# Performance work log

Measured on AMD Instinct MI355X. Metric: run time of the kernel, lower is better.

Reference implementation:

```python
import jax, jax.numpy as jnp
import numpy as np

# Mamba hyperparams (mamba_ssm defaults for d_model=128)
D_MODEL = 128
DEPTH = 8
D_INNER = 256   # expand=2
D_STATE = 16
D_CONV = 4
DT_RANK = 8     # ceil(D_MODEL/16)
EPS = 1e-5


def setup_inputs() -> dict:
    key = jax.random.key(0)
    ks = jax.random.split(key, 8)
    B, H, W = 1, 48, 48
    s = lambda k, shape, sc=0.02: jax.random.normal(k, shape, jnp.float32) * sc
    return {
        "x": jax.random.normal(ks[0], (B, D_MODEL, H, W), jnp.float32),
        "W_in": s(ks[1], (DEPTH, D_MODEL, 2 * D_INNER)),
        "conv_w": s(ks[2], (DEPTH, D_INNER, D_CONV), 0.2),
        "conv_b": jnp.zeros((DEPTH, D_INNER), jnp.float32),
        "W_xproj": s(ks[3], (DEPTH, D_INNER, DT_RANK + 2 * D_STATE)),
        "W_dt": s(ks[4], (DEPTH, DT_RANK, D_INNER), 0.1),
        "b_dt": jnp.full((DEPTH, D_INNER), -4.6, jnp.float32),  # softplus ~= 0.01
        "A_log": jnp.broadcast_to(
            jnp.log(jnp.arange(1, D_STATE + 1, dtype=jnp.float32)),
            (DEPTH, D_INNER, D_STATE)).copy(),
        "D_skip": jnp.ones((DEPTH, D_INNER), jnp.float32),
        "W_out": s(ks[5], (DEPTH, D_INNER, D_MODEL)),
        "rms_w": jnp.ones((DEPTH, D_MODEL), jnp.float32),
    }


def _rmsnorm(x, w):
    return x * jax.lax.rsqrt(jnp.mean(x * x, axis=-1, keepdims=True) + EPS) * w


def _mamba_layer(x, Wi, cw, cb, Wx, Wdt, bdt, Alog, Dp, Wo):
    # x: [B, L, D_MODEL]
    B, L, _ = x.shape
    xz = x @ Wi                                   # [B, L, 2*d_inner]
    xi, z = jnp.split(xz, 2, axis=-1)
    # causal depthwise conv1d, kernel D_CONV
    xp = jnp.pad(xi, ((0, 0), (D_CONV - 1, 0), (0, 0)))
    xc = sum(xp[:, k:k + L, :] * cw[:, k] for k in range(D_CONV)) + cb
    xc = jax.nn.silu(xc)                          # [B, L, d_inner]
    dbl = xc @ Wx                                 # [B, L, dt_rank + 2*d_state]
    dt_r = dbl[..., :DT_RANK]
    Bs = dbl[..., DT_RANK:DT_RANK + D_STATE]      # [B, L, d_state]
    Cs = dbl[..., DT_RANK + D_STATE:]
    dt = jax.nn.softplus(dt_r @ Wdt + bdt)        # [B, L, d_inner]
    A = -jnp.exp(Alog)                            # [d_inner, d_state]
    dA = jnp.exp(dt[..., None] * A)               # [B, L, d_inner, d_state]
    dBx = (dt * xc)[..., None] * Bs[:, :, None, :]
    # linear recurrence h_t = dA_t * h_{t-1} + dBx_t via parallel scan
    def comb(l, r):
        al, bl = l
        ar, br = r
        return ar * al, ar * bl + br
    _, h = jax.lax.associative_scan(comb, (dA, dBx), axis=1)
    y = jnp.einsum('blds,bls->bld', h, Cs) + Dp * xc
    y = y * jax.nn.silu(z)
    return y @ Wo                                 # [B, L, D_MODEL]


def reference(x, W_in, conv_w, conv_b, W_xproj, W_dt, b_dt, A_log, D_skip, W_out, rms_w):
    B, C, H, W = x.shape
    seq = x.reshape(B, C, H * W).transpose(0, 2, 1)  # [B, L, C]
    for l in range(DEPTH):
        seq = _mamba_layer(seq, W_in[l], conv_w[l], conv_b[l], W_xproj[l],
                           W_dt[l], b_dt[l], A_log[l], D_skip[l], W_out[l])
        seq = _rmsnorm(seq, rms_w[l])
    return seq.reshape(B, H, W, C).transpose(0, 3, 1, 2)
```

## Files before the change

### kernel.cpp

```cpp
#include <hip/hip_runtime.h>
#include <math.h>

#define LSEQ 2304
#define DM 128
#define DI 256
#define DS 16
#define RK 8
#define NCH 576
#define CLEN 4
#define NG 24
#define GS 24
#define NSI (DI*DS)
#define EPSF 1e-5f

__device__ __forceinline__ float silu_f(float s) { return s / (1.f + __expf(-s)); }
__device__ __forceinline__ float softplus_f(float x) { return (x > 20.f) ? x : log1pf(__expf(x)); }

template<bool FIRST>
__global__ __launch_bounds__(256, 4)
void k_in(const float* __restrict__ seq, const float* __restrict__ x0,
          const float* __restrict__ Wi,
          const float* __restrict__ cw, const float* __restrict__ cbias,
          float* __restrict__ xc_g, float* __restrict__ sz_g) {
    __shared__ float As[19 * 128];
    const int l0 = blockIdx.x * 16;
    const int half = blockIdx.y & 1;
    const bool isZ = blockIdx.y >= 2;
    const int tid = threadIdx.x;

    if (FIRST) {
        const int rlo = isZ ? 3 : 0;
        for (int idx = tid + rlo * 128; idx < 19 * 128; idx += 256) {
            const int r = idx >> 7, cc = idx & 127;
            const int l = l0 - 3 + r;
            As[idx] = (l >= 0) ? x0[cc * LSEQ + l] : 0.f;
        }
    } else if (!isZ) {
        for (int idx = tid; idx < 19 * 32; idx += 256) {
            const int r = idx >> 5, cq = (idx & 31) * 4;
            const int l = l0 - 3 + r;
            const float4 v = (l >= 0) ? *(const float4*)&seq[l * DM + cq]
                                      : make_float4(0.f, 0.f, 0.f, 0.f);
            *(float4*)&As[r * 128 + cq] = v;
        }
    } else {
        for (int idx = tid; idx < 16 * 32; idx += 256) {
            const int r = 3 + (idx >> 5), cq = (idx & 31) * 4;
            *(float4*)&As[r * 128 + cq] =
                *(const float4*)&seq[(l0 - 3 + r) * DM + cq];
        }
    }
    __syncthreads();

    const int c = tid & 127;
    const int rg = tid >> 7;
    const int d = half * 128 + c;

    if (!isZ) {
        float ax[11];
#pragma unroll
        for (int r = 0; r < 11; ++r) ax[r] = 0.f;
        for (int k4 = 0; k4 < 32; ++k4) {
            float bv[4];
#pragma unroll
            for (int u = 0; u < 4; ++u) bv[u] = Wi[(k4 * 4 + u) * 512 + d];
#pragma unroll
            for (int r = 0; r < 11; ++r) {
                const float4 a4 = *(const float4*)&As[(rg * 8 + r) * 128 + k4 * 4];
                ax[r] += a4.x * bv[0] + a4.y * bv[1] + a4.z * bv[2] + a4.w * bv[3];
            }
        }
        const float w0 = cw[d * 4 + 0], w1 = cw[d * 4 + 1];
        const float w2 = cw[d * 4 + 2], w3 = cw[d * 4 + 3];
        const float cbv = cbias[d];
#pragma unroll
        for (int rr = 0; rr < 8; ++rr) {
            const float v = silu_f(cbv + w0 * ax[rr] + w1 * ax[rr + 1] +
                                   w2 * ax[rr + 2] + w3 * ax[rr + 3]);
            xc_g[(l0 + rg * 8 + rr) * DI + d] = v;
        }
    } else {
        float az[8];
#pragma unroll
        for (int r = 0; r < 8; ++r) az[r] = 0.f;
        for (int k4 = 0; k4 < 32; ++k4) {
            float bv[4];
#pragma unroll
            for (int u = 0; u < 4; ++u) bv[u] = Wi[(k4 * 4 + u) * 512 + 256 + d];
#pragma unroll
            for (int r = 0; r < 8; ++r) {
                const float4 a4 = *(const float4*)&As[(rg * 8 + r + 3) * 128 + k4 * 4];
                az[r] += a4.x * bv[0] + a4.y * bv[1] + a4.z * bv[2] + a4.w * bv[3];
            }
        }
#pragma unroll
        for (int rr = 0; rr < 8; ++rr)
            sz_g[(l0 + rg * 8 + rr) * DI + d] = silu_f(az[rr]);
    }
}

__global__ __launch_bounds__(256, 4)
void k_mid2(const float* __restrict__ xc_g,
            const float* __restrict__ Wx,
            const float* __restrict__ Wdt, const float* __restrict__ bdt,
            const float* __restrict__ Alog,
            float* __restrict__ dbl_g, float* __restrict__ dts_g,
            float* __restrict__ S) {
    __shared__ float xcs[CLEN * 256];
    __shared__ float part[4 * 160];
    __shared__ float dtrs[CLEN * 8];
    __shared__ float dbls[CLEN * 32];
    const int c = blockIdx.x;
    const int l0 = c * CLEN;
    const int tid = threadIdx.x;
    const int d = tid;

    ((float4*)xcs)[tid] = ((const float4*)&xc_g[l0 * DI])[tid];
    __syncthreads();

    for (int task = tid; task < 640; task += 256) {
        const int kc = task / 160;
        const int o = task - kc * 160;
        const int r = o / 40, j = o - r * 40;
        const float* xr = &xcs[r * 256 + kc * 64];
        const float* wp = &Wx[(kc * 64) * 40 + j];
        float acc = 0.f;
#pragma unroll 8
        for (int k = 0; k < 64; ++k) acc += xr[k] * wp[k * 40];
        part[kc * 160 + o] = acc;
    }
    __syncthreads();
    if (tid < 160) {
        const float acc = part[tid] + part[160 + tid] + part[320 + tid] + part[480 + tid];
        const int r = tid / 40, j = tid - r * 40;
        dbl_g[(l0 + r) * 40 + j] = acc;
        if (j < RK) dtrs[r * 8 + j] = acc;
        else dbls[r * 32 + (j - 8)] = acc;
    }
    __syncthreads();

    float dtv[CLEN], xcv[CLEN];
    {
        float wdt[8];
#pragma unroll
        for (int q = 0; q < 8; ++q) wdt[q] = Wdt[q * DI + d];
        const float bdv = bdt[d];
#pragma unroll
        for (int r = 0; r < CLEN; ++r) {
            float acc = bdv;
#pragma unroll
            for (int q = 0; q < 8; ++q) acc += dtrs[r * 8 + q] * wdt[q];
            dtv[r] = softplus_f(acc);
            xcv[r] = xcs[r * 256 + d];
        }
    }
    dts_g[c * DI + d] = dtv[0] + dtv[1] + dtv[2] + dtv[3];

    float A[16], hs[16];
#pragma unroll
    for (int v = 0; v < 4; ++v) {
        const float4 a4 = *(const float4*)&Alog[d * DS + v * 4];
        A[v * 4 + 0] = -__expf(a4.x);
        A[v * 4 + 1] = -__expf(a4.y);
        A[v * 4 + 2] = -__expf(a4.z);
        A[v * 4 + 3] = -__expf(a4.w);
    }
#pragma unroll
    for (int s = 0; s < 16; ++s) hs[s] = 0.f;
#pragma unroll
    for (int t = 0; t < CLEN; ++t) {
        const float dtt = dtv[t];
        const float uv = dtt * xcv[t];
        const float* Brow = &dbls[t * 32];
#pragma unroll
        for (int s = 0; s < 16; ++s) {
            const float e = __expf(dtt * A[s]);
            hs[s] = e * hs[s] + uv * Brow[s];
        }
    }
    const int base = c * NSI + d * DS;
#pragma unroll
    for (int v = 0; v < 4; ++v) {
        *(float4*)&S[base + v * 4] =
            make_float4(hs[v * 4], hs[v * 4 + 1], hs[v * 4 + 2], hs[v * 4 + 3]);
    }
}

__global__ __launch_bounds__(256, 4)
void k_carry1(float* __restrict__ S, const float* __restrict__ dts,
              const float* __restrict__ Alog,
              float* __restrict__ dtspre,
              float* __restrict__ Pg, float* __restrict__ Sg) {
    const int g = blockIdx.x;
    const int i = blockIdx.y * 256 + threadIdx.x;
    const int d = i >> 4;
    const float Av = -__expf(Alog[i]);
    float G = 0.f, cd = 0.f;
    const int base = g * GS * NSI + i;
    const int c0 = g * GS;
#pragma unroll 8
    for (int k = 0; k < GS; ++k) {
        const int idx = base + k * NSI;
        const float dtsv = dts[(c0 + k) * DI + d];
        if ((i & 15) == 0) dtspre[(c0 + k) * DI + d] = cd;
        const float p = __expf(Av * dtsv);
        const float s = S[idx];
        S[idx] = G;
        G = p * G + s;
        cd += dtsv;
    }
    Pg[g * NSI + i] = __expf(Av * cd);
    Sg[g * NSI + i] = G;
}

__global__ __launch_bounds__(256, 4)
void k_carry2(const float* __restrict__ Pg, float* __restrict__ Sg) {
    const int i = blockIdx.x * 256 + threadIdx.x;
    float G = 0.f;
#pragma unroll 8
    for (int g = 0; g < NG; ++g) {
        const int idx = g * NSI + i;
        const float p = Pg[idx];
        const float s = Sg[idx];
        Sg[idx] = G;
        G = p * G + s;
    }
}

template<bool LAST>
__global__ __launch_bounds__(256, 3)
void k_tail(const float* __restrict__ xc_g, const float* __restrict__ dbl_g,
            const float* __restrict__ Alog, const float* __restrict__ Sloc,
            const float* __restrict__ dtspre, const float* __restrict__ Gc,
            const float* __restrict__ Dp, const float* __restrict__ sz_g,
            const float* __restrict__ Wdt, const float* __restrict__ bdt,
            const float* __restrict__ Wo, const float* __restrict__ rmsw,
            float* __restrict__ seq, float* __restrict__ out) {
    __shared__ float dbls[CLEN * 40];
    __shared__ float Ys[CLEN * 256];
    __shared__ float partO[4 * CLEN * 128];
    __shared__ float Os[CLEN * 129];
    __shared__ float red[CLEN * 32];
    __shared__ float scaleS[CLEN];
    const int c = blockIdx.x;
    const int g = c / GS;
    const int l0 = c * CLEN;
    const int tid = threadIdx.x;
    const int d = tid;

    if (tid < CLEN * 40) dbls[tid] = dbl_g[l0 * 40 + tid];

    float A[16], h[16];
    const float cdts = dtspre[c * DI + d];
#pragma unroll
    for (int v = 0; v < 4; ++v) {
        const float4 a4 = *(const float4*)&Alog[d * DS + v * 4];
        A[v * 4 + 0] = -__expf(a4.x);
        A[v * 4 + 1] = -__expf(a4.y);
        A[v * 4 + 2] = -__expf(a4.z);
        A[v * 4 + 3] = -__expf(a4.w);
        const float4 s4 = *(const float4*)&Sloc[c * NSI + d * DS + v * 4];
        const float4 g4 = *(const float4*)&Gc[g * NSI + d * DS + v * 4];
        h[v * 4 + 0] = s4.x + __expf(A[v * 4 + 0] * cdts) * g4.x;
        h[v * 4 + 1] = s4.y + __expf(A[v * 4 + 1] * cdts) * g4.y;
        h[v * 4 + 2] = s4.z + __expf(A[v * 4 + 2] * cdts) * g4.z;
        h[v * 4 + 3] = s4.w + __expf(A[v * 4 + 3] * cdts) * g4.w;
    }
    float xcv[CLEN], szv[CLEN];
#pragma unroll
    for (int r = 0; r < CLEN; ++r) {
        xcv[r] = xc_g[(l0 + r) * DI + d];
        szv[r] = sz_g[(l0 + r) * DI + d];
    }
    const float dskip = Dp[d];
    __syncthreads();

    float dtv[CLEN];
    {
        float wdt[8];
#pragma unroll
        for (int q = 0; q < 8; ++q) wdt[q] = Wdt[q * DI + d];
        const float bdv = bdt[d];
#pragma unroll
        for (int r = 0; r < CLEN; ++r) {
            float acc = bdv;
#pragma unroll
            for (int q = 0; q < 8; ++q) acc += dbls[r * 40 + q] * wdt[q];
            dtv[r] = softplus_f(acc);
        }
    }
#pragma unroll
    for (int t = 0; t < CLEN; ++t) {
        const float dtt = dtv[t];
        const float uv = dtt * xcv[t];
        const float* Brow = &dbls[t * 40 + 8];
        const float* Crow = &dbls[t * 40 + 24];
        float sum = 0.f;
#pragma unroll
        for (int s = 0; s < 16; ++s) {
            const float e = __expf(dtt * A[s]);
            h[s] = e * h[s] + uv * Brow[s];
            sum += h[s] * Crow[s];
        }
        Ys[t * 256 + d] = (sum + dskip * xcv[t]) * szv[t];
    }
    __syncthreads();

    {
        const int ccp = tid & 63;
        const int kg = tid >> 6;
        float acc[CLEN][2];
#pragma unroll
        for (int r = 0; r < CLEN; ++r) { acc[r][0] = 0.f; acc[r][1] = 0.f; }
        const float* wp = &Wo[(kg * 64) * DM + ccp * 2];
        const float* yp = &Ys[kg * 64];
#pragma unroll 8
        for (int k = 0; k < 64; ++k) {
            const float2 w2 = *(const float2*)(wp + k * DM);
#pragma unroll
            for (int r = 0; r < CLEN; ++r) {
                const float yv = yp[r * 256 + k];
                acc[r][0] += yv * w2.x;
                acc[r][1] += yv * w2.y;
            }
        }
#pragma unroll
        for (int r = 0; r < CLEN; ++r) {
            partO[(kg * CLEN + r) * 128 + ccp * 2 + 0] = acc[r][0];
            partO[(kg * CLEN + r) * 128 + ccp * 2 + 1] = acc[r][1];
        }
        __syncthreads();
        for (int idx = tid; idx < CLEN * 128; idx += 256) {
            const int r = idx >> 7, cc = idx & 127;
            Os[r * 129 + cc] = partO[(0 * CLEN + r) * 128 + cc] +
                               partO[(1 * CLEN + r) * 128 + cc] +
                               partO[(2 * CLEN + r) * 128 + cc] +
                               partO[(3 * CLEN + r) * 128 + cc];
        }
        __syncthreads();
    }

    if (tid < CLEN * 32) {
        const int r = tid >> 5, part = tid & 31;
        float ss = 0.f;
#pragma unroll
        for (int i = 0; i < 4; ++i) {
            const float v = Os[r * 129 + part * 4 + i];
            ss += v * v;
        }
        red[tid] = ss;
    }
    __syncthreads();
    if (tid < CLEN) {
        float ss = 0.f;
#pragma unroll
        for (int p = 0; p < 32; ++p) ss += red[tid * 32 + p];
        scaleS[tid] = rsqrtf(ss * (1.f / DM) + EPSF);
    }
    __syncthreads();
    if (LAST) {
        for (int idx = tid; idx < CLEN * DM; idx += 256) {
            const int r = idx >> 7, cc = idx & 127;
            out[cc * LSEQ + (l0 + r)] = Os[r * 129 + cc] * scaleS[r] * rmsw[cc];
        }
    } else {
        for (int idx = tid; idx < CLEN * DM; idx += 256) {
            const int r = idx >> 7, cc = idx & 127;
            seq[(l0 + r) * DM + cc] = Os[r * 129 + cc] * scaleS[r] * rmsw[cc];
        }
    }
}

extern "C" void kernel_launch(void* const* d_in, const int* in_sizes, int n_in,
                              void* d_out, int out_size, void* d_ws, size_t ws_size,
                              hipStream_t stream) {
    const float* x    = (const float*)d_in[0];
    const float* W_in = (const float*)d_in[1];
    const float* cw   = (const float*)d_in[2];
    const float* cb   = (const float*)d_in[3];
    const float* Wx   = (const float*)d_in[4];
    const float* Wdt  = (const float*)d_in[5];
    const float* bdt  = (const float*)d_in[6];
    const float* Alog = (const float*)d_in[7];
    const float* Dp   = (const float*)d_in[8];
    const float* Wo   = (const float*)d_in[9];
    const float* rmsw = (const float*)d_in[10];
    float* out = (float*)d_out;

    float* ws      = (float*)d_ws;
    float* seq     = ws; ws += LSEQ * DM;
    float* szb     = ws; ws += LSEQ * DI;
    float* xcb     = ws; ws += LSEQ * DI;
    float* dblb    = ws; ws += LSEQ * 40;
    float* dtsb    = ws; ws += NCH * DI;
    float* dtspreb = ws; ws += NCH * DI;
    float* Sb      = ws; ws += NCH * NSI;
    float* Pgb     = ws; ws += NG * NSI;
    float* Sgb     = ws; ws += NG * NSI;

    for (int layer = 0; layer < 8; ++layer) {
        const float* Wi_l   = W_in + (size_t)layer * DM * 512;
        const float* cw_l   = cw   + (size_t)layer * DI * 4;
        const float* cb_l   = cb   + (size_t)layer * DI;
        const float* Wx_l   = Wx   + (size_t)layer * DI * 40;
        const float* Wdt_l  = Wdt  + (size_t)layer * RK * DI;
        const float* bdt_l  = bdt  + (size_t)layer * DI;
        const float* Alog_l = Alog + (size_t)layer * DI * DS;
        const float* Dp_l   = Dp   + (size_t)layer * DI;
        const float* Wo_l   = Wo   + (size_t)layer * DI * DM;
        const float* rmsw_l = rmsw + (size_t)layer * DM;

        if (layer == 0)
            k_in<true><<<dim3(144, 4), 256, 0, stream>>>(seq, x, Wi_l, cw_l, cb_l,
                                                         xcb, szb);
        else
            k_in<false><<<dim3(144, 4), 256, 0, stream>>>(seq, x, Wi_l, cw_l, cb_l,
                                                          xcb, szb);

        k_mid2<<<NCH, 256, 0, stream>>>(xcb, Wx_l, Wdt_l, bdt_l, Alog_l,
                                        dblb, dtsb, Sb);

        k_carry1<<<dim3(NG, 16), 256, 0, stream>>>(Sb, dtsb, Alog_l,
                                                   dtspreb, Pgb, Sgb);
        k_carry2<<<16, 256, 0, stream>>>(Pgb, Sgb);

        if (layer == 7)
            k_tail<true><<<NCH, 256, 0, stream>>>(xcb, dblb, Alog_l, Sb, dtspreb,
                                                  Sgb, Dp_l, szb, Wdt_l, bdt_l,
                                                  Wo_l, rmsw_l, seq, out);
        else
            k_tail<false><<<NCH, 256, 0, stream>>>(xcb, dblb, Alog_l, Sb, dtspreb,
                                                   Sgb, Dp_l, szb, Wdt_l, bdt_l,
                                                   Wo_l, rmsw_l, seq, out);
    }
}
```

Before: 574.8 us.

## Fuse input projection with chunk-scan front, drop carry2 by folding group prefix into tail

```diff
diff --git a/kernel.cpp b/kernel.cpp
--- a/kernel.cpp
+++ b/kernel.cpp
@@ -8,9 +8,11 @@
 #define RK 8
 #define NCH 576
 #define CLEN 4
-#define NG 24
-#define GS 24
+#define NG 8
+#define GS 72
 #define NSI (DI*DS)
+#define TROWS 8
+#define NT (LSEQ/TROWS)
 #define EPSF 1e-5f
 
 __device__ __forceinline__ float silu_f(float s) { return s / (1.f + __expf(-s)); }
@@ -18,25 +20,36 @@
 
 template<bool FIRST>
 __global__ __launch_bounds__(256, 4)
-void k_in(const float* __restrict__ seq, const float* __restrict__ x0,
-          const float* __restrict__ Wi,
-          const float* __restrict__ cw, const float* __restrict__ cbias,
-          float* __restrict__ xc_g, float* __restrict__ sz_g) {
-    __shared__ float As[19 * 128];
-    const int l0 = blockIdx.x * 16;
-    const int half = blockIdx.y & 1;
-    const bool isZ = blockIdx.y >= 2;
+void k_front(const float* __restrict__ seq, const float* __restrict__ x0,
+             const float* __restrict__ Wi,
+             const float* __restrict__ cw, const float* __restrict__ cbias,
+             const float* __restrict__ Wx,
+             const float* __restrict__ Wdt, const float* __restrict__ bdt,
+             const float* __restrict__ Alog,
+             float* __restrict__ xc_g, float* __restrict__ sz_g,
+             float* __restrict__ dbl_g, float* __restrict__ dts_g,
+             float* __restrict__ S) {
+    __shared__ float As[11 * 128];
+    __shared__ float xcs[TROWS * 256];
+    __shared__ float part[2 * 4 * 160];
+    __shared__ float dtrs[TROWS * 8];
+    __shared__ float dbls[TROWS * 32];
+
+    const int tile = blockIdx.x;
+    const int l0 = tile * TROWS;
+    const bool isZ = blockIdx.y == 1;
     const int tid = threadIdx.x;
+    const int d = tid;
 
     if (FIRST) {
         const int rlo = isZ ? 3 : 0;
-        for (int idx = tid + rlo * 128; idx < 19 * 128; idx += 256) {
+        for (int idx = tid + rlo * 128; idx < 11 * 128; idx += 256) {
             const int r = idx >> 7, cc = idx & 127;
             const int l = l0 - 3 + r;
             As[idx] = (l >= 0) ? x0[cc * LSEQ + l] : 0.f;
         }
     } else if (!isZ) {
-        for (int idx = tid; idx < 19 * 32; idx += 256) {
+        for (int idx = tid; idx < 11 * 32; idx += 256) {
             const int r = idx >> 5, cq = (idx & 31) * 4;
             const int l = l0 - 3 + r;
             const float4 v = (l >= 0) ? *(const float4*)&seq[l * DM + cq]
@@ -44,7 +57,7 @@
             *(float4*)&As[r * 128 + cq] = v;
         }
     } else {
-        for (int idx = tid; idx < 16 * 32; idx += 256) {
+        for (int idx = tid; idx < 8 * 32; idx += 256) {
             const int r = 3 + (idx >> 5), cq = (idx & 31) * 4;
             *(float4*)&As[r * 128 + cq] =
                 *(const float4*)&seq[(l0 - 3 + r) * DM + cq];
@@ -52,24 +65,40 @@
     }
     __syncthreads();
 
-    const int c = tid & 127;
-    const int rg = tid >> 7;
-    const int d = half * 128 + c;
-
-    if (!isZ) {
-        float ax[11];
-#pragma unroll
-        for (int r = 0; r < 11; ++r) ax[r] = 0.f;
+    if (isZ) {
+        float az[8];
+#pragma unroll
+        for (int r = 0; r < 8; ++r) az[r] = 0.f;
         for (int k4 = 0; k4 < 32; ++k4) {
             float bv[4];
 #pragma unroll
-            for (int u = 0; u < 4; ++u) bv[u] = Wi[(k4 * 4 + u) * 512 + d];
-#pragma unroll
-            for (int r = 0; r < 11; ++r) {
-                const float4 a4 = *(const float4*)&As[(rg * 8 + r) * 128 + k4 * 4];
-                ax[r] += a4.x * bv[0] + a4.y * bv[1] + a4.z * bv[2] + a4.w * bv[3];
+            for (int u = 0; u < 4; ++u) bv[u] = Wi[(k4 * 4 + u) * 512 + 256 + d];
+#pragma unroll
+            for (int r = 0; r < 8; ++r) {
+                const float4 a4 = *(const float4*)&As[(r + 3) * 128 + k4 * 4];
+                az[r] += a4.x * bv[0] + a4.y * bv[1] + a4.z * bv[2] + a4.w * bv[3];
             }
         }
+#pragma unroll
+        for (int rr = 0; rr < 8; ++rr)
+            sz_g[(l0 + rr) * DI + d] = silu_f(az[rr]);
+        return;
+    }
+
+    float ax[11];
+#pragma unroll
+    for (int r = 0; r < 11; ++r) ax[r] = 0.f;
+    for (int k4 = 0; k4 < 32; ++k4) {
+        float bv[4];
+#pragma unroll
+        for (int u = 0; u < 4; ++u) bv[u] = Wi[(k4 * 4 + u) * 512 + d];
+#pragma unroll
+        for (int r = 0; r < 11; ++r) {
+            const float4 a4 = *(const float4*)&As[r * 128 + k4 * 4];
+            ax[r] += a4.x * bv[0] + a4.y * bv[1] + a4.z * bv[2] + a4.w * bv[3];
+        }
+    }
+    {
         const float w0 = cw[d * 4 + 0], w1 = cw[d * 4 + 1];
         const float w2 = cw[d * 4 + 2], w3 = cw[d * 4 + 3];
         const float cbv = cbias[d];
@@ -77,86 +106,42 @@
         for (int rr = 0; rr < 8; ++rr) {
             const float v = silu_f(cbv + w0 * ax[rr] + w1 * ax[rr + 1] +
                                    w2 * ax[rr + 2] + w3 * ax[rr + 3]);
-            xc_g[(l0 + rg * 8 + rr) * DI + d] = v;
-        }
-    } else {
-        float az[8];
-#pragma unroll
-        for (int r = 0; r < 8; ++r) az[r] = 0.f;
-        for (int k4 = 0; k4 < 32; ++k4) {
-            float bv[4];
-#pragma unroll
-            for (int u = 0; u < 4; ++u) bv[u] = Wi[(k4 * 4 + u) * 512 + 256 + d];
-#pragma unroll
-            for (int r = 0; r < 8; ++r) {
-                const float4 a4 = *(const float4*)&As[(rg * 8 + r + 3) * 128 + k4 * 4];
-                az[r] += a4.x * bv[0] + a4.y * bv[1] + a4.z * bv[2] + a4.w * bv[3];
-            }
-        }
-#pragma unroll
-        for (int rr = 0; rr < 8; ++rr)
-            sz_g[(l0 + rg * 8 + rr) * DI + d] = silu_f(az[rr]);
-    }
-}
-
-__global__ __launch_bounds__(256, 4)
-void k_mid2(const float* __restrict__ xc_g,
-            const float* __restrict__ Wx,
-            const float* __restrict__ Wdt, const float* __restrict__ bdt,
-            const float* __restrict__ Alog,
-            float* __restrict__ dbl_g, float* __restrict__ dts_g,
-            float* __restrict__ S) {
-    __shared__ float xcs[CLEN * 256];
-    __shared__ float part[4 * 160];
-    __shared__ float dtrs[CLEN * 8];
-    __shared__ float dbls[CLEN * 32];
-    const int c = blockIdx.x;
-    const int l0 = c * CLEN;
-    const int tid = threadIdx.x;
-    const int d = tid;
-
-    ((float4*)xcs)[tid] = ((const float4*)&xc_g[l0 * DI])[tid];
-    __syncthreads();
-
-    for (int task = tid; task < 640; task += 256) {
-        const int kc = task / 160;
-        const int o = task - kc * 160;
+            xcs[rr * 256 + d] = v;
+            xc_g[(l0 + rr) * DI + d] = v;
+        }
+    }
+    __syncthreads();
+
+    for (int task = tid; task < 1280; task += 256) {
+        const int q = task / 640;
+        const int rem = task - q * 640;
+        const int kc = rem / 160;
+        const int o = rem - kc * 160;
         const int r = o / 40, j = o - r * 40;
-        const float* xr = &xcs[r * 256 + kc * 64];
+        const float* xr = &xcs[(q * 4 + r) * 256 + kc * 64];
         const float* wp = &Wx[(kc * 64) * 40 + j];
         float acc = 0.f;
 #pragma unroll 8
         for (int k = 0; k < 64; ++k) acc += xr[k] * wp[k * 40];
-        part[kc * 160 + o] = acc;
-    }
-    __syncthreads();
-    if (tid < 160) {
-        const float acc = part[tid] + part[160 + tid] + part[320 + tid] + part[480 + tid];
-        const int r = tid / 40, j = tid - r * 40;
-        dbl_g[(l0 + r) * 40 + j] = acc;
-        if (j < RK) dtrs[r * 8 + j] = acc;
-        else dbls[r * 32 + (j - 8)] = acc;
-    }
-    __syncthreads();
-
-    float dtv[CLEN], xcv[CLEN];
-    {
-        float wdt[8];
-#pragma unroll
-        for (int q = 0; q < 8; ++q) wdt[q] = Wdt[q * DI + d];
-        const float bdv = bdt[d];
-#pragma unroll
-        for (int r = 0; r < CLEN; ++r) {
-            float acc = bdv;
-#pragma unroll
-            for (int q = 0; q < 8; ++q) acc += dtrs[r * 8 + q] * wdt[q];
-            dtv[r] = softplus_f(acc);
-            xcv[r] = xcs[r * 256 + d];
-        }
-    }
-    dts_g[c * DI + d] = dtv[0] + dtv[1] + dtv[2] + dtv[3];
-
-    float A[16], hs[16];
+        part[(q * 4 + kc) * 160 + o] = acc;
+    }
+    __syncthreads();
+    for (int idx = tid; idx < 320; idx += 256) {
+        const int q = idx / 160, o = idx - q * 160;
+        const float acc = part[(q * 4 + 0) * 160 + o] + part[(q * 4 + 1) * 160 + o] +
+                          part[(q * 4 + 2) * 160 + o] + part[(q * 4 + 3) * 160 + o];
+        const int r = o / 40, j = o - r * 40;
+        dbl_g[(l0 + q * 4 + r) * 40 + j] = acc;
+        if (j < RK) dtrs[(q * 4 + r) * 8 + j] = acc;
+        else        dbls[(q * 4 + r) * 32 + (j - 8)] = acc;
+    }
+    __syncthreads();
+
+    float wdt[8];
+#pragma unroll
+    for (int q8 = 0; q8 < 8; ++q8) wdt[q8] = Wdt[q8 * DI + d];
+    const float bdv = bdt[d];
+    float A[16];
 #pragma unroll
     for (int v = 0; v < 4; ++v) {
         const float4 a4 = *(const float4*)&Alog[d * DS + v * 4];
@@ -166,38 +151,54 @@
         A[v * 4 + 3] = -__expf(a4.w);
     }
 #pragma unroll
-    for (int s = 0; s < 16; ++s) hs[s] = 0.f;
-#pragma unroll
-    for (int t = 0; t < CLEN; ++t) {
-        const float dtt = dtv[t];
-        const float uv = dtt * xcv[t];
-        const float* Brow = &dbls[t * 32];
-#pragma unroll
-        for (int s = 0; s < 16; ++s) {
-            const float e = __expf(dtt * A[s]);
-            hs[s] = e * hs[s] + uv * Brow[s];
-        }
-    }
-    const int base = c * NSI + d * DS;
-#pragma unroll
-    for (int v = 0; v < 4; ++v) {
-        *(float4*)&S[base + v * 4] =
-            make_float4(hs[v * 4], hs[v * 4 + 1], hs[v * 4 + 2], hs[v * 4 + 3]);
+    for (int q = 0; q < 2; ++q) {
+        const int c = tile * 2 + q;
+        float dtv[CLEN], xcv[CLEN];
+#pragma unroll
+        for (int r = 0; r < CLEN; ++r) {
+            float acc = bdv;
+#pragma unroll
+            for (int k = 0; k < 8; ++k) acc += dtrs[(q * 4 + r) * 8 + k] * wdt[k];
+            dtv[r] = softplus_f(acc);
+            xcv[r] = xcs[(q * 4 + r) * 256 + d];
+        }
+        dts_g[c * DI + d] = dtv[0] + dtv[1] + dtv[2] + dtv[3];
+
+        float hs[16];
+#pragma unroll
+        for (int s = 0; s < 16; ++s) hs[s] = 0.f;
+#pragma unroll
+        for (int t = 0; t < CLEN; ++t) {
+            const float dtt = dtv[t];
+            const float uv = dtt * xcv[t];
+            const float* Brow = &dbls[(q * 4 + t) * 32];
+#pragma unroll
+            for (int s = 0; s < 16; ++s) {
+                const float e = __expf(dtt * A[s]);
+                hs[s] = e * hs[s] + uv * Brow[s];
+            }
+        }
+        const int base = c * NSI + d * DS;
+#pragma unroll
+        for (int v = 0; v < 4; ++v) {
+            *(float4*)&S[base + v * 4] =
+                make_float4(hs[v * 4], hs[v * 4 + 1], hs[v * 4 + 2], hs[v * 4 + 3]);
+        }
     }
 }
 
 __global__ __launch_bounds__(256, 4)
-void k_carry1(float* __restrict__ S, const float* __restrict__ dts,
-              const float* __restrict__ Alog,
-              float* __restrict__ dtspre,
-              float* __restrict__ Pg, float* __restrict__ Sg) {
+void k_carry(float* __restrict__ S, const float* __restrict__ dts,
+             const float* __restrict__ Alog,
+             float* __restrict__ dtspre,
+             float* __restrict__ Pg, float* __restrict__ Sg) {
     const int g = blockIdx.x;
     const int i = blockIdx.y * 256 + threadIdx.x;
     const int d = i >> 4;
     const float Av = -__expf(Alog[i]);
     float G = 0.f, cd = 0.f;
-    const int base = g * GS * NSI + i;
     const int c0 = g * GS;
+    const int base = c0 * NSI + i;
 #pragma unroll 8
     for (int k = 0; k < GS; ++k) {
         const int idx = base + k * NSI;
@@ -213,25 +214,12 @@
     Sg[g * NSI + i] = G;
 }
 
-__global__ __launch_bounds__(256, 4)
-void k_carry2(const float* __restrict__ Pg, float* __restrict__ Sg) {
-    const int i = blockIdx.x * 256 + threadIdx.x;
-    float G = 0.f;
-#pragma unroll 8
-    for (int g = 0; g < NG; ++g) {
-        const int idx = g * NSI + i;
-        const float p = Pg[idx];
-        const float s = Sg[idx];
-        Sg[idx] = G;
-        G = p * G + s;
-    }
-}
-
 template<bool LAST>
 __global__ __launch_bounds__(256, 3)
 void k_tail(const float* __restrict__ xc_g, const float* __restrict__ dbl_g,
             const float* __restrict__ Alog, const float* __restrict__ Sloc,
-            const float* __restrict__ dtspre, const float* __restrict__ Gc,
+            const float* __restrict__ dtspre,
+            const float* __restrict__ Pg, const float* __restrict__ Sg,
             const float* __restrict__ Dp, const float* __restrict__ sz_g,
             const float* __restrict__ Wdt, const float* __restrict__ bdt,
             const float* __restrict__ Wo, const float* __restrict__ rmsw,
@@ -251,7 +239,6 @@
     if (tid < CLEN * 40) dbls[tid] = dbl_g[l0 * 40 + tid];
 
     float A[16], h[16];
-    const float cdts = dtspre[c * DI + d];
 #pragma unroll
     for (int v = 0; v < 4; ++v) {
         const float4 a4 = *(const float4*)&Alog[d * DS + v * 4];
@@ -259,12 +246,28 @@
         A[v * 4 + 1] = -__expf(a4.y);
         A[v * 4 + 2] = -__expf(a4.z);
         A[v * 4 + 3] = -__expf(a4.w);
+    }
+#pragma unroll
+    for (int s = 0; s < 16; ++s) h[s] = 0.f;
+    for (int gp = 0; gp < g; ++gp) {
+#pragma unroll
+        for (int v = 0; v < 4; ++v) {
+            const float4 p4 = *(const float4*)&Pg[gp * NSI + d * DS + v * 4];
+            const float4 s4 = *(const float4*)&Sg[gp * NSI + d * DS + v * 4];
+            h[v * 4 + 0] = p4.x * h[v * 4 + 0] + s4.x;
+            h[v * 4 + 1] = p4.y * h[v * 4 + 1] + s4.y;
+            h[v * 4 + 2] = p4.z * h[v * 4 + 2] + s4.z;
+            h[v * 4 + 3] = p4.w * h[v * 4 + 3] + s4.w;
+        }
+    }
+    const float cdts = dtspre[c * DI + d];
+#pragma unroll
+    for (int v = 0; v < 4; ++v) {
         const float4 s4 = *(const float4*)&Sloc[c * NSI + d * DS + v * 4];
-        const float4 g4 = *(const float4*)&Gc[g * NSI + d * DS + v * 4];
-        h[v * 4 + 0] = s4.x + __expf(A[v * 4 + 0] * cdts) * g4.x;
-        h[v * 4 + 1] = s4.y + __expf(A[v * 4 + 1] * cdts) * g4.y;
-        h[v * 4 + 2] = s4.z + __expf(A[v * 4 + 2] * cdts) * g4.z;
-        h[v * 4 + 3] = s4.w + __expf(A[v * 4 + 3] * cdts) * g4.w;
+        h[v * 4 + 0] = s4.x + __expf(A[v * 4 + 0] * cdts) * h[v * 4 + 0];
+        h[v * 4 + 1] = s4.y + __expf(A[v * 4 + 1] * cdts) * h[v * 4 + 1];
+        h[v * 4 + 2] = s4.z + __expf(A[v * 4 + 2] * cdts) * h[v * 4 + 2];
+        h[v * 4 + 3] = s4.w + __expf(A[v * 4 + 3] * cdts) * h[v * 4 + 3];
     }
     float xcv[CLEN], szv[CLEN];
 #pragma unroll
@@ -411,26 +414,24 @@
         const float* rmsw_l = rmsw + (size_t)layer * DM;
 
         if (layer == 0)
-            k_in<true><<<dim3(144, 4), 256, 0, stream>>>(seq, x, Wi_l, cw_l, cb_l,
-                                                         xcb, szb);
+            k_front<true><<<dim3(NT, 2), 256, 0, stream>>>(seq, x, Wi_l, cw_l, cb_l,
+                                                           Wx_l, Wdt_l, bdt_l, Alog_l,
+                                                           xcb, szb, dblb, dtsb, Sb);
         else
-            k_in<false><<<dim3(144, 4), 256, 0, stream>>>(seq, x, Wi_l, cw_l, cb_l,
-                                                          xcb, szb);
-
-        k_mid2<<<NCH, 256, 0, stream>>>(xcb, Wx_l, Wdt_l, bdt_l, Alog_l,
-                                        dblb, dtsb, Sb);
-
-        k_carry1<<<dim3(NG, 16), 256, 0, stream>>>(Sb, dtsb, Alog_l,
-                                                   dtspreb, Pgb, Sgb);
-        k_carry2<<<16, 256, 0, stream>>>(Pgb, Sgb);
+            k_front<false><<<dim3(NT, 2), 256, 0, stream>>>(seq, x, Wi_l, cw_l, cb_l,
+                                                            Wx_l, Wdt_l, bdt_l, Alog_l,
+                                                            xcb, szb, dblb, dtsb, Sb);
+
+        k_carry<<<dim3(NG, 16), 256, 0, stream>>>(Sb, dtsb, Alog_l,
+                                                  dtspreb, Pgb, Sgb);
 
         if (layer == 7)
             k_tail<true><<<NCH, 256, 0, stream>>>(xcb, dblb, Alog_l, Sb, dtspreb,
-                                                  Sgb, Dp_l, szb, Wdt_l, bdt_l,
+                                                  Pgb, Sgb, Dp_l, szb, Wdt_l, bdt_l,
                                                   Wo_l, rmsw_l, seq, out);
         else
             k_tail<false><<<NCH, 256, 0, stream>>>(xcb, dblb, Alog_l, Sb, dtspreb,
-                                                   Sgb, Dp_l, szb, Wdt_l, bdt_l,
+                                                   Pgb, Sgb, Dp_l, szb, Wdt_l, bdt_l,
                                                    Wo_l, rmsw_l, seq, out);
     }
 }
```

Measured after the change: 671.7 us. 1.17x slower.
